# Optimization experiments

Measured on AMD Instinct MI355X. Metric: run time of the kernel, lower is better.

The kernel has to match this reference:

```python
import jax, jax.numpy as jnp
import numpy as np

INPUT_SIZE = 128
OUTPUT_SIZE = 32
LIFTING_DIM = 512
BATCH = 32768


def setup_inputs() -> dict:
    key = jax.random.key(0)
    ks = jax.random.split(key, 7)
    x = jax.random.normal(ks[0], (BATCH, INPUT_SIZE), dtype=jnp.float32)
    # Linear(input_size, lifting_dim) with bias (torch layout: W [out, in])
    lim1 = 1.0 / np.sqrt(INPUT_SIZE)
    W1 = jax.random.uniform(ks[1], (LIFTING_DIM, INPUT_SIZE), jnp.float32, -lim1, lim1)
    b1 = jax.random.uniform(ks[2], (LIFTING_DIM,), jnp.float32, -lim1, lim1)
    # Linear(lifting_dim, output_size, bias=False)
    lim2 = 1.0 / np.sqrt(LIFTING_DIM)
    W2 = jax.random.uniform(ks[3], (OUTPUT_SIZE, LIFTING_DIM), jnp.float32, -lim2, lim2)
    # Quadratic params: L_vars ~ randn, b ~ randn, c ~ randn (as in module init)
    n_tril = LIFTING_DIM * (LIFTING_DIM + 1) // 2
    L_vars = jax.random.normal(ks[4], (n_tril,), dtype=jnp.float32)
    qb = jax.random.normal(ks[5], (LIFTING_DIM,), dtype=jnp.float32)
    qc = jax.random.normal(ks[6], (1,), dtype=jnp.float32)
    return {"x": x, "W1": W1, "b1": b1, "W2": W2, "L_vars": L_vars, "qb": qb, "qc": qc}


def reference(x, W1, b1, W2, L_vars, qb, qc):
    # lifting: phi = tanh(x @ W1^T + b1)   [B, lifting_dim]
    phi = jnp.tanh(x @ W1.T + b1)
    # actor: linear feedback (no bias)     [B, output_size]
    pi = phi @ W2.T
    # critic: quadratic form y = phi' Q phi + b' phi + c with Q = L L^T (PSD)
    rows, cols = jnp.tril_indices(LIFTING_DIM)  # row-major, same order as torch.tril_indices
    L = jnp.zeros((LIFTING_DIM, LIFTING_DIM), dtype=L_vars.dtype).at[rows, cols].set(L_vars)
    Q = L @ L.T
    # diag(phi @ Q @ phi.T) == sum((phi @ Q) * phi, axis=1)  -- O(B*d^2), same math
    y = jnp.sum((phi @ Q) * phi, axis=1) + phi @ qb + qc  # [B]
    vf = y[:, None]  # [B, 1]
    return pi, vf
```

## Files before the change

kernel.cpp:

```cpp
#include <hip/hip_runtime.h>
#include <hip/hip_bf16.h>
#include <stdint.h>

typedef short bf16x8 __attribute__((ext_vector_type(8)));
typedef float f32x4 __attribute__((ext_vector_type(4)));

#define DEVI static __device__ __forceinline__

constexpr int B_   = 32768;
constexpr int IN_  = 128;
constexpr int LF_  = 512;
constexpr int OUT_ = 32;
constexpr int NE_  = 48;

constexpr size_t OFF_XB  = 0;
constexpr size_t OFF_PHI = 8388608;
constexpr size_t OFF_LT  = OFF_PHI + 33554432;
constexpr size_t OFF_W1  = OFF_LT + 524288;
constexpr size_t OFF_W2E = OFF_W1 + 131072;

DEVI void gl2lds16(const void* g, void* l) {
    __builtin_amdgcn_global_load_lds(
        (const __attribute__((address_space(1))) unsigned int*)g,
        (__attribute__((address_space(3))) unsigned int*)l,
        16, 0, 0);
}

DEVI void stage128x64(const __hip_bfloat16* src, int ld, char* lds, int tid) {
    int wv = tid >> 6;
    char* base = lds + (size_t)(wv * 64) * 16;
#pragma unroll
    for (int it = 0; it < 4; ++it) {
        int slot = it * 256 + tid;
        int row  = slot >> 3;
        int c    = (slot & 7) ^ (row & 7);
        gl2lds16(src + (size_t)row * ld + c * 8, base + it * 256 * 16);
    }
}

DEVI bf16x8 fragLD(const char* lds, int row, int kofs) {
    int c    = kofs >> 3;
    int slot = row * 8 + ((c ^ (row & 7)));
    return *(const bf16x8*)(lds + (size_t)slot * 16);
}

__global__ __launch_bounds__(256) void k_prep(
        const float* __restrict__ x,  const float* __restrict__ w1,
        const float* __restrict__ w2, const float* __restrict__ lv,
        const float* __restrict__ qb,
        __hip_bfloat16* __restrict__ xb, __hip_bfloat16* __restrict__ w1b,
        __hip_bfloat16* __restrict__ lt, __hip_bfloat16* __restrict__ w2e) {
    int gt = blockIdx.x * blockDim.x + threadIdx.x;
    int st = gridDim.x * blockDim.x;
    for (int i = gt; i < B_ * IN_; i += st) xb[i] = __float2bfloat16(x[i]);
    for (int i = gt; i < LF_ * IN_; i += st) w1b[i] = __float2bfloat16(w1[i]);
    for (int i = gt; i < NE_ * LF_; i += st) {
        int n = i >> 9, k = i & 511;
        float v = (n < OUT_) ? w2[n * LF_ + k] : (n == OUT_ ? qb[k] : 0.f);
        w2e[i] = __float2bfloat16(v);
    }
    for (int i = gt; i < LF_ * LF_; i += st) {
        int j = i >> 9, k = i & 511;
        float v = (k >= j) ? lv[k * (k + 1) / 2 + j] : 0.f;
        lt[i] = __float2bfloat16(v);
    }
}

__global__ __launch_bounds__(256) void k_phi(
        const __hip_bfloat16* __restrict__ xb, const __hip_bfloat16* __restrict__ w1,
        const float* __restrict__ b1, __hip_bfloat16* __restrict__ phi) {
    __shared__ char As[16384];
    __shared__ char Bs[16384];
    int tid = threadIdx.x;
    int m0 = blockIdx.x * 128, n0 = blockIdx.y * 128;
    int wv = tid >> 6, ln = tid & 63;
    int wm = (wv & 1) * 64, wn = (wv >> 1) * 64;
    int cl = ln & 15, q = ln >> 4;
    f32x4 acc[4][4] = {};
    for (int k0 = 0; k0 < IN_; k0 += 64) {
        stage128x64(xb + (size_t)m0 * IN_ + k0, IN_, As, tid);
        stage128x64(w1 + (size_t)n0 * IN_ + k0, IN_, Bs, tid);
        __syncthreads();
#pragma unroll
        for (int kk = 0; kk < 64; kk += 32) {
            bf16x8 af[4], bf[4];
#pragma unroll
            for (int i = 0; i < 4; ++i) af[i] = fragLD(As, wm + i * 16 + cl, kk + q * 8);
#pragma unroll
            for (int i = 0; i < 4; ++i) bf[i] = fragLD(Bs, wn + i * 16 + cl, kk + q * 8);
#pragma unroll
            for (int mi = 0; mi < 4; ++mi)
#pragma unroll
                for (int ni = 0; ni < 4; ++ni)
                    acc[mi][ni] = __builtin_amdgcn_mfma_f32_16x16x32_bf16(
                        af[mi], bf[ni], acc[mi][ni], 0, 0, 0);
        }
        __syncthreads();
    }
#pragma unroll
    for (int ni = 0; ni < 4; ++ni) {
        int col = n0 + wn + ni * 16 + cl;
        float bv = b1[col];
#pragma unroll
        for (int mi = 0; mi < 4; ++mi)
#pragma unroll
            for (int r = 0; r < 4; ++r) {
                int row = m0 + wm + mi * 16 + q * 4 + r;
                phi[(size_t)row * LF_ + col] = __float2bfloat16(tanhf(acc[mi][ni][r] + bv));
            }
    }
}

__global__ __launch_bounds__(256) void k_pi(
        const __hip_bfloat16* __restrict__ phi, const __hip_bfloat16* __restrict__ w2e,
        const float* __restrict__ qcp, float* __restrict__ pi, float* __restrict__ vf) {
    __shared__ char As[16384];
    __shared__ char Bs[49152];
    int tid = threadIdx.x;
    int m0 = blockIdx.x * 128;
    int wv = tid >> 6, ln = tid & 63;
    int cl = ln & 15, q = ln >> 4;
    {
        char* base = Bs + (size_t)(wv * 64) * 16;
#pragma unroll
        for (int it = 0; it < 12; ++it) {
            int slot = it * 256 + tid;
            int n = slot >> 6;
            int c = (slot & 63) ^ (n & 7);
            gl2lds16(w2e + (size_t)n * LF_ + c * 8, base + it * 256 * 16);
        }
    }
    f32x4 acc[2][3] = {};
    for (int k0 = 0; k0 < LF_; k0 += 64) {
        stage128x64(phi + (size_t)m0 * LF_ + k0, LF_, As, tid);
        __syncthreads();
#pragma unroll
        for (int kk = 0; kk < 64; kk += 32) {
            bf16x8 af[2], bf[3];
#pragma unroll
            for (int i = 0; i < 2; ++i) af[i] = fragLD(As, wv * 32 + i * 16 + cl, kk + q * 8);
#pragma unroll
            for (int i = 0; i < 3; ++i) {
                int n = i * 16 + cl;
                int C = (k0 + kk) / 8 + q;
                int slot = n * 64 + (C ^ (n & 7));
                bf[i] = *(const bf16x8*)(Bs + (size_t)slot * 16);
            }
#pragma unroll
            for (int mi = 0; mi < 2; ++mi)
#pragma unroll
                for (int ni = 0; ni < 3; ++ni)
                    acc[mi][ni] = __builtin_amdgcn_mfma_f32_16x16x32_bf16(
                        af[mi], bf[ni], acc[mi][ni], 0, 0, 0);
        }
        __syncthreads();
    }
    float qc0 = qcp[0];
#pragma unroll
    for (int mi = 0; mi < 2; ++mi)
#pragma unroll
        for (int r = 0; r < 4; ++r) {
            int row = m0 + wv * 32 + mi * 16 + q * 4 + r;
#pragma unroll
            for (int ni = 0; ni < 3; ++ni) {
                float v = acc[mi][ni][r];
                int col = ni * 16 + cl;
                if (col < OUT_)      pi[(size_t)row * OUT_ + col] = v;
                else if (col == OUT_) vf[row] = v + qc0;
            }
        }
}

__global__ __launch_bounds__(256) void k_y(
        const __hip_bfloat16* __restrict__ phi, const __hip_bfloat16* __restrict__ lt,
        float* __restrict__ vf) {
    __shared__ char As[16384];
    __shared__ char Bs[16384];
    int tid = threadIdx.x;
    int m0 = blockIdx.x * 128, n0 = blockIdx.y * 128;
    int wv = tid >> 6, ln = tid & 63;
    int wm = (wv & 1) * 64, wn = (wv >> 1) * 64;
    int cl = ln & 15, q = ln >> 4;
    f32x4 acc[4][4] = {};
    for (int k0 = n0; k0 < LF_; k0 += 64) {
        stage128x64(phi + (size_t)m0 * LF_ + k0, LF_, As, tid);
        stage128x64(lt  + (size_t)n0 * LF_ + k0, LF_, Bs, tid);
        __syncthreads();
#pragma unroll
        for (int kk = 0; kk < 64; kk += 32) {
            bf16x8 af[4], bf[4];
#pragma unroll
            for (int i = 0; i < 4; ++i) af[i] = fragLD(As, wm + i * 16 + cl, kk + q * 8);
#pragma unroll
            for (int i = 0; i < 4; ++i) bf[i] = fragLD(Bs, wn + i * 16 + cl, kk + q * 8);
#pragma unroll
            for (int mi = 0; mi < 4; ++mi)
#pragma unroll
                for (int ni = 0; ni < 4; ++ni)
                    acc[mi][ni] = __builtin_amdgcn_mfma_f32_16x16x32_bf16(
                        af[mi], bf[ni], acc[mi][ni], 0, 0, 0);
        }
        __syncthreads();
    }
#pragma unroll
    for (int mi = 0; mi < 4; ++mi)
#pragma unroll
        for (int r = 0; r < 4; ++r) {
            float v = 0.f;
#pragma unroll
            for (int ni = 0; ni < 4; ++ni) { float t = acc[mi][ni][r]; v += t * t; }
            v += __shfl_xor(v, 1, 64);
            v += __shfl_xor(v, 2, 64);
            v += __shfl_xor(v, 4, 64);
            v += __shfl_xor(v, 8, 64);
            if (cl == 0) atomicAdd(&vf[m0 + wm + mi * 16 + q * 4 + r], v);
        }
}

extern "C" void kernel_launch(void* const* d_in, const int* in_sizes, int n_in,
                              void* d_out, int out_size, void* d_ws, size_t ws_size,
                              hipStream_t stream) {
    const float* x  = (const float*)d_in[0];
    const float* w1 = (const float*)d_in[1];
    const float* b1 = (const float*)d_in[2];
    const float* w2 = (const float*)d_in[3];
    const float* lv = (const float*)d_in[4];
    const float* qb = (const float*)d_in[5];
    const float* qc = (const float*)d_in[6];

    char* ws = (char*)d_ws;
    __hip_bfloat16* xb  = (__hip_bfloat16*)(ws + OFF_XB);
    __hip_bfloat16* phi = (__hip_bfloat16*)(ws + OFF_PHI);
    __hip_bfloat16* lt  = (__hip_bfloat16*)(ws + OFF_LT);
    __hip_bfloat16* w1b = (__hip_bfloat16*)(ws + OFF_W1);
    __hip_bfloat16* w2e = (__hip_bfloat16*)(ws + OFF_W2E);

    float* pi = (float*)d_out;
    float* vf = pi + (size_t)B_ * OUT_;

    k_prep<<<1024, 256, 0, stream>>>(x, w1, w2, lv, qb, xb, w1b, lt, w2e);
    k_phi<<<dim3(B_ / 128, LF_ / 128), 256, 0, stream>>>(xb, w1b, b1, phi);
    k_pi <<<B_ / 128, 256, 0, stream>>>(phi, w2e, qc, pi, vf);
    k_y  <<<dim3(B_ / 128, LF_ / 128), 256, 0, stream>>>(phi, lt, vf);
}
```

Baseline: 128.2 us.

## Fuse phi, actor and critic GEMMs into one kernel with phi kept in LDS

Result: no change. 128.2 us (+0.0%).

```diff
diff --git a/kernel.cpp b/kernel.cpp
--- a/kernel.cpp
+++ b/kernel.cpp
@@ -14,8 +14,7 @@
 constexpr int NE_  = 48;
 
 constexpr size_t OFF_XB  = 0;
-constexpr size_t OFF_PHI = 8388608;
-constexpr size_t OFF_LT  = OFF_PHI + 33554432;
+constexpr size_t OFF_LT  = 8388608;
 constexpr size_t OFF_W1  = OFF_LT + 524288;
 constexpr size_t OFF_W2E = OFF_W1 + 131072;
 
@@ -26,22 +25,17 @@
         16, 0, 0);
 }
 
-DEVI void stage128x64(const __hip_bfloat16* src, int ld, char* lds, int tid) {
-    int wv = tid >> 6;
-    char* base = lds + (size_t)(wv * 64) * 16;
-#pragma unroll
-    for (int it = 0; it < 4; ++it) {
-        int slot = it * 256 + tid;
-        int row  = slot >> 3;
-        int c    = (slot & 7) ^ (row & 7);
-        gl2lds16(src + (size_t)row * ld + c * 8, base + it * 256 * 16);
-    }
-}
-
-DEVI bf16x8 fragLD(const char* lds, int row, int kofs) {
-    int c    = kofs >> 3;
-    int slot = row * 8 + ((c ^ (row & 7)));
-    return *(const bf16x8*)(lds + (size_t)slot * 16);
+DEVI bf16x8 frag4(const char* base, int row, int kofs) {
+    int c = ((kofs >> 3) & 3) ^ (row & 3);
+    return *(const bf16x8*)(base + (size_t)((row << 2) + c) * 16);
+}
+DEVI bf16x8 phiFrag(const char* p, int row, int kofs) {
+    int c = (kofs >> 3) ^ (row & 7);
+    return *(const bf16x8*)(p + (size_t)((row << 6) + c) * 16);
+}
+DEVI void phiStore(char* p, int row, int col, __hip_bfloat16 v) {
+    int c = (col >> 3) ^ (row & 7);
+    *(__hip_bfloat16*)(p + (size_t)((row << 6) + c) * 16 + (col & 7) * 2) = v;
 }
 
 __global__ __launch_bounds__(256) void k_prep(
@@ -66,155 +60,151 @@
     }
 }
 
-__global__ __launch_bounds__(256) void k_phi(
-        const __hip_bfloat16* __restrict__ xb, const __hip_bfloat16* __restrict__ w1,
-        const float* __restrict__ b1, __hip_bfloat16* __restrict__ phi) {
-    __shared__ char As[16384];
-    __shared__ char Bs[16384];
-    int tid = threadIdx.x;
-    int m0 = blockIdx.x * 128, n0 = blockIdx.y * 128;
-    int wv = tid >> 6, ln = tid & 63;
-    int wm = (wv & 1) * 64, wn = (wv >> 1) * 64;
-    int cl = ln & 15, q = ln >> 4;
-    f32x4 acc[4][4] = {};
-    for (int k0 = 0; k0 < IN_; k0 += 64) {
-        stage128x64(xb + (size_t)m0 * IN_ + k0, IN_, As, tid);
-        stage128x64(w1 + (size_t)n0 * IN_ + k0, IN_, Bs, tid);
-        __syncthreads();
-#pragma unroll
-        for (int kk = 0; kk < 64; kk += 32) {
-            bf16x8 af[4], bf[4];
-#pragma unroll
-            for (int i = 0; i < 4; ++i) af[i] = fragLD(As, wm + i * 16 + cl, kk + q * 8);
-#pragma unroll
-            for (int i = 0; i < 4; ++i) bf[i] = fragLD(Bs, wn + i * 16 + cl, kk + q * 8);
+__global__ __launch_bounds__(256, 2) void k_fused(
+        const __hip_bfloat16* __restrict__ xb, const __hip_bfloat16* __restrict__ w1b,
+        const float* __restrict__ b1, const __hip_bfloat16* __restrict__ w2e,
+        const __hip_bfloat16* __restrict__ lt, const float* __restrict__ qcp,
+        float* __restrict__ pi, float* __restrict__ vf) {
+    __shared__ char smem[79104];
+    char*  phiB   = smem;
+    char*  stageA = smem + 65536;
+    char*  stageB = smem + 69632;
+    float* vfb    = (float*)(smem + 77824);
+    float* vfp    = (float*)(smem + 78080);
+
+    const int tid = threadIdx.x, wv = tid >> 6, ln = tid & 63;
+    const int cl = ln & 15, q = ln >> 4;
+    const int m0 = blockIdx.x * 64;
+
+    {
+        const int wm = (wv & 1) * 32, wn = (wv >> 1) * 64;
+        for (int n0 = 0; n0 < LF_; n0 += 128) {
+            f32x4 acc[2][4] = {};
+            for (int k0 = 0; k0 < IN_; k0 += 32) {
+                __syncthreads();
+                {
+                    int slot = tid, row = slot >> 2, c = (slot & 3) ^ (row & 3);
+                    gl2lds16(xb + (size_t)(m0 + row) * IN_ + k0 + c * 8,
+                             stageA + (size_t)(wv * 64) * 16);
+                }
+#pragma unroll
+                for (int it = 0; it < 2; ++it) {
+                    int slot = it * 256 + tid, row = slot >> 2, c = (slot & 3) ^ (row & 3);
+                    gl2lds16(w1b + (size_t)(n0 + row) * IN_ + k0 + c * 8,
+                             stageB + (size_t)(it * 256 + wv * 64) * 16);
+                }
+                __syncthreads();
+                bf16x8 af[2], bfr[4];
+#pragma unroll
+                for (int i = 0; i < 2; ++i) af[i]  = frag4(stageA, wm + i * 16 + cl, q * 8);
+#pragma unroll
+                for (int i = 0; i < 4; ++i) bfr[i] = frag4(stageB, wn + i * 16 + cl, q * 8);
+#pragma unroll
+                for (int mi = 0; mi < 2; ++mi)
+#pragma unroll
+                    for (int ni = 0; ni < 4; ++ni)
+                        acc[mi][ni] = __builtin_amdgcn_mfma_f32_16x16x32_bf16(
+                            af[mi], bfr[ni], acc[mi][ni], 0, 0, 0);
+            }
+#pragma unroll
+            for (int ni = 0; ni < 4; ++ni) {
+                int colg = n0 + wn + ni * 16 + cl;
+                float bv = b1[colg];
+#pragma unroll
+                for (int mi = 0; mi < 2; ++mi)
+#pragma unroll
+                    for (int r = 0; r < 4; ++r) {
+                        int row = wm + mi * 16 + q * 4 + r;
+                        phiStore(phiB, row, colg,
+                                 __float2bfloat16(tanhf(acc[mi][ni][r] + bv)));
+                    }
+            }
+        }
+    }
+    __syncthreads();
+
+    {
+        const int wm = wv * 16;
+        f32x4 a2[3] = {};
+        for (int k0 = 0; k0 < LF_; k0 += 32) {
+            bf16x8 a = phiFrag(phiB, wm + cl, k0 + q * 8);
+#pragma unroll
+            for (int ni = 0; ni < 3; ++ni) {
+                bf16x8 b = *(const bf16x8*)(w2e + (size_t)(ni * 16 + cl) * LF_ + k0 + q * 8);
+                a2[ni] = __builtin_amdgcn_mfma_f32_16x16x32_bf16(a, b, a2[ni], 0, 0, 0);
+            }
+        }
+#pragma unroll
+        for (int ni = 0; ni < 3; ++ni)
+#pragma unroll
+            for (int r = 0; r < 4; ++r) {
+                int row = wm + q * 4 + r, col = ni * 16 + cl;
+                float v = a2[ni][r];
+                if (col < OUT_)       pi[(size_t)(m0 + row) * OUT_ + col] = v;
+                else if (col == OUT_) vfb[row] = v;
+            }
+    }
+
+    {
+        const int wn = wv * 32;
+        float vacc[4][4] = {};
+        for (int n0 = 0; n0 < LF_; n0 += 128) {
+            f32x4 acc[4][2] = {};
+            for (int k0 = n0; k0 < LF_; k0 += 32) {
+                __syncthreads();
+#pragma unroll
+                for (int it = 0; it < 2; ++it) {
+                    int slot = it * 256 + tid, row = slot >> 2, c = (slot & 3) ^ (row & 3);
+                    gl2lds16(lt + (size_t)(n0 + row) * LF_ + k0 + c * 8,
+                             stageB + (size_t)(it * 256 + wv * 64) * 16);
+                }
+                __syncthreads();
+                bf16x8 bfr[2];
+#pragma unroll
+                for (int ni = 0; ni < 2; ++ni) bfr[ni] = frag4(stageB, wn + ni * 16 + cl, q * 8);
+#pragma unroll
+                for (int mi = 0; mi < 4; ++mi) {
+                    bf16x8 a = phiFrag(phiB, mi * 16 + cl, k0 + q * 8);
+#pragma unroll
+                    for (int ni = 0; ni < 2; ++ni)
+                        acc[mi][ni] = __builtin_amdgcn_mfma_f32_16x16x32_bf16(
+                            a, bfr[ni], acc[mi][ni], 0, 0, 0);
+                }
+            }
 #pragma unroll
             for (int mi = 0; mi < 4; ++mi)
 #pragma unroll
-                for (int ni = 0; ni < 4; ++ni)
-                    acc[mi][ni] = __builtin_amdgcn_mfma_f32_16x16x32_bf16(
-                        af[mi], bf[ni], acc[mi][ni], 0, 0, 0);
+                for (int r = 0; r < 4; ++r) {
+                    float s = 0.f;
+#pragma unroll
+                    for (int ni = 0; ni < 2; ++ni) { float t = acc[mi][ni][r]; s += t * t; }
+                    vacc[mi][r] += s;
+                }
         }
-        __syncthreads();
-    }
-#pragma unroll
-    for (int ni = 0; ni < 4; ++ni) {
-        int col = n0 + wn + ni * 16 + cl;
-        float bv = b1[col];
 #pragma unroll
         for (int mi = 0; mi < 4; ++mi)
 #pragma unroll
             for (int r = 0; r < 4; ++r) {
-                int row = m0 + wm + mi * 16 + q * 4 + r;
-                phi[(size_t)row * LF_ + col] = __float2bfloat16(tanhf(acc[mi][ni][r] + bv));
-            }
-    }
-}
-
-__global__ __launch_bounds__(256) void k_pi(
-        const __hip_bfloat16* __restrict__ phi, const __hip_bfloat16* __restrict__ w2e,
-        const float* __restrict__ qcp, float* __restrict__ pi, float* __restrict__ vf) {
-    __shared__ char As[16384];
-    __shared__ char Bs[49152];
-    int tid = threadIdx.x;
-    int m0 = blockIdx.x * 128;
-    int wv = tid >> 6, ln = tid & 63;
-    int cl = ln & 15, q = ln >> 4;
-    {
-        char* base = Bs + (size_t)(wv * 64) * 16;
-#pragma unroll
-        for (int it = 0; it < 12; ++it) {
-            int slot = it * 256 + tid;
-            int n = slot >> 6;
-            int c = (slot & 63) ^ (n & 7);
-            gl2lds16(w2e + (size_t)n * LF_ + c * 8, base + it * 256 * 16);
-        }
-    }
-    f32x4 acc[2][3] = {};
-    for (int k0 = 0; k0 < LF_; k0 += 64) {
-        stage128x64(phi + (size_t)m0 * LF_ + k0, LF_, As, tid);
-        __syncthreads();
-#pragma unroll
-        for (int kk = 0; kk < 64; kk += 32) {
-            bf16x8 af[2], bf[3];
-#pragma unroll
-            for (int i = 0; i < 2; ++i) af[i] = fragLD(As, wv * 32 + i * 16 + cl, kk + q * 8);
-#pragma unroll
-            for (int i = 0; i < 3; ++i) {
-                int n = i * 16 + cl;
-                int C = (k0 + kk) / 8 + q;
-                int slot = n * 64 + (C ^ (n & 7));
-                bf[i] = *(const bf16x8*)(Bs + (size_t)slot * 16);
-            }
-#pragma unroll
-            for (int mi = 0; mi < 2; ++mi)
-#pragma unroll
-                for (int ni = 0; ni < 3; ++ni)
-                    acc[mi][ni] = __builtin_amdgcn_mfma_f32_16x16x32_bf16(
-                        af[mi], bf[ni], acc[mi][ni], 0, 0, 0);
-        }
-        __syncthreads();
-    }
-    float qc0 = qcp[0];
-#pragma unroll
-    for (int mi = 0; mi < 2; ++mi)
-#pragma unroll
-        for (int r = 0; r < 4; ++r) {
-            int row = m0 + wv * 32 + mi * 16 + q * 4 + r;
-#pragma unroll
-            for (int ni = 0; ni < 3; ++ni) {
-                float v = acc[mi][ni][r];
-                int col = ni * 16 + cl;
-                if (col < OUT_)      pi[(size_t)row * OUT_ + col] = v;
-                else if (col == OUT_) vf[row] = v + qc0;
-            }
-        }
-}
-
-__global__ __launch_bounds__(256) void k_y(
-        const __hip_bfloat16* __restrict__ phi, const __hip_bfloat16* __restrict__ lt,
-        float* __restrict__ vf) {
-    __shared__ char As[16384];
-    __shared__ char Bs[16384];
-    int tid = threadIdx.x;
-    int m0 = blockIdx.x * 128, n0 = blockIdx.y * 128;
-    int wv = tid >> 6, ln = tid & 63;
-    int wm = (wv & 1) * 64, wn = (wv >> 1) * 64;
-    int cl = ln & 15, q = ln >> 4;
-    f32x4 acc[4][4] = {};
-    for (int k0 = n0; k0 < LF_; k0 += 64) {
-        stage128x64(phi + (size_t)m0 * LF_ + k0, LF_, As, tid);
-        stage128x64(lt  + (size_t)n0 * LF_ + k0, LF_, Bs, tid);
-        __syncthreads();
-#pragma unroll
-        for (int kk = 0; kk < 64; kk += 32) {
-            bf16x8 af[4], bf[4];
-#pragma unroll
-            for (int i = 0; i < 4; ++i) af[i] = fragLD(As, wm + i * 16 + cl, kk + q * 8);
-#pragma unroll
-            for (int i = 0; i < 4; ++i) bf[i] = fragLD(Bs, wn + i * 16 + cl, kk + q * 8);
+                float v = vacc[mi][r];
+                v += __shfl_xor(v, 1, 64);
+                v += __shfl_xor(v, 2, 64);
+                v += __shfl_xor(v, 4, 64);
+                v += __shfl_xor(v, 8, 64);
+                vacc[mi][r] = v;
+            }
+        if (cl == 0)
 #pragma unroll
             for (int mi = 0; mi < 4; ++mi)
 #pragma unroll
-                for (int ni = 0; ni < 4; ++ni)
-                    acc[mi][ni] = __builtin_amdgcn_mfma_f32_16x16x32_bf16(
-                        af[mi], bf[ni], acc[mi][ni], 0, 0, 0);
-        }
-        __syncthreads();
-    }
-#pragma unroll
-    for (int mi = 0; mi < 4; ++mi)
-#pragma unroll
-        for (int r = 0; r < 4; ++r) {
-            float v = 0.f;
-#pragma unroll
-            for (int ni = 0; ni < 4; ++ni) { float t = acc[mi][ni][r]; v += t * t; }
-            v += __shfl_xor(v, 1, 64);
-            v += __shfl_xor(v, 2, 64);
-            v += __shfl_xor(v, 4, 64);
-            v += __shfl_xor(v, 8, 64);
-            if (cl == 0) atomicAdd(&vf[m0 + wm + mi * 16 + q * 4 + r], v);
-        }
+                for (int r = 0; r < 4; ++r)
+                    vfp[wv * 64 + mi * 16 + q * 4 + r] = vacc[mi][r];
+    }
+    __syncthreads();
+    if (tid < 64) {
+        float v = vfb[tid] + qcp[0] +
+                  vfp[tid] + vfp[64 + tid] + vfp[128 + tid] + vfp[192 + tid];
+        vf[m0 + tid] = v;
+    }
 }
 
 extern "C" void kernel_launch(void* const* d_in, const int* in_sizes, int n_in,
@@ -230,7 +220,6 @@
 
     char* ws = (char*)d_ws;
     __hip_bfloat16* xb  = (__hip_bfloat16*)(ws + OFF_XB);
-    __hip_bfloat16* phi = (__hip_bfloat16*)(ws + OFF_PHI);
     __hip_bfloat16* lt  = (__hip_bfloat16*)(ws + OFF_LT);
     __hip_bfloat16* w1b = (__hip_bfloat16*)(ws + OFF_W1);
     __hip_bfloat16* w2e = (__hip_bfloat16*)(ws + OFF_W2E);
@@ -238,8 +227,6 @@
     float* pi = (float*)d_out;
     float* vf = pi + (size_t)B_ * OUT_;
 
-    k_prep<<<1024, 256, 0, stream>>>(x, w1, w2, lv, qb, xb, w1b, lt, w2e);
-    k_phi<<<dim3(B_ / 128, LF_ / 128), 256, 0, stream>>>(xb, w1b, b1, phi);
-    k_pi <<<B_ / 128, 256, 0, stream>>>(phi, w2e, qc, pi, vf);
-    k_y  <<<dim3(B_ / 128, LF_ / 128), 256, 0, stream>>>(phi, lt, vf);
-}
+    k_prep <<<1024, 256, 0, stream>>>(x, w1, w2, lv, qb, xb, w1b, lt, w2e);
+    k_fused<<<B_ / 64, 256, 0, stream>>>(xb, w1b, b1, w2e, lt, qc, pi, vf);
+}
```
